# Kernel tuning notes

Hardware: AMD Instinct MI355X
Metric: run time of the kernel (lower is better)

Reference implementation:

```python
import jax, jax.numpy as jnp
import numpy as np
import math

B, C, N, L = 32, 128, 2048, 1
H, DK, APT = 8, 16, 10
EPS = 1e-5


def conv1x1(x, W, b):
    # 1x1 Conv2d on [B, C, N, L]
    return jnp.einsum('oc,bcnl->bonl', W, x) + b[None, :, None, None]


def layer_norm_12(x):
    # normalize over dims (1, 2) as in the custom LayerNorm (no affine)
    mean = x.mean(axis=(1, 2), keepdims=True)
    var = x.var(axis=(1, 2), keepdims=True)
    return (x - mean) / jnp.sqrt(var + EPS)


def setup_inputs() -> dict:
    key = jax.random.key(0)
    ks = jax.random.split(key, 10)
    s = 0.05  # small-scale init for numerical stability
    inp = {
        'input': jax.random.normal(ks[0], (B, C, N, L), jnp.float32),
        'Wq': jax.random.normal(ks[1], (C, C), jnp.float32) * s,
        'bq': jnp.zeros((C,), jnp.float32),
        'Wv': jax.random.normal(ks[2], (C, C), jnp.float32) * s,
        'bv': jnp.zeros((C,), jnp.float32),
        'Wc': jax.random.normal(ks[3], (C, C), jnp.float32) * s,
        'bc': jnp.zeros((C,), jnp.float32),
        'memory': jax.random.normal(ks[4], (H, L, N, DK), jnp.float32) * s,
        'sa_weight': jnp.ones((C, N, L), jnp.float32),
        'sa_bias': jnp.zeros((C, N, L), jnp.float32),
        'nodevec1': jax.random.normal(ks[5], (N, APT), jnp.float32),
        'nodevec2': jax.random.normal(ks[6], (APT, N), jnp.float32),
        'Wg1': jax.random.normal(ks[7], (C, C), jnp.float32) * s,
        'bg1': jnp.zeros((C,), jnp.float32),
        'Wg2': jax.random.normal(ks[8], (C, C), jnp.float32) * s,
        'bg2': jnp.zeros((C,), jnp.float32),
        'Wg3': jax.random.normal(ks[9], (C, C), jnp.float32) * s,
        'bg3': jnp.zeros((C,), jnp.float32),
    }
    return inp


def reference(input, Wq, bq, Wv, bv, Wc, bc, memory, sa_weight, sa_bias,
              nodevec1, nodevec2, Wg1, bg1, Wg2, bg2, Wg3, bg3):
    scale = math.sqrt(DK)

    def split_heads(t):  # [B,C,N,L] -> [B,H,L,N,DK]
        return t.reshape(B, H, DK, N, L).transpose(0, 1, 4, 3, 2)

    # SpatialAttention (Conv = 1x1 conv + relu; dropout off in eval)
    q = jax.nn.relu(conv1x1(input, Wq, bq))
    v = jax.nn.relu(conv1x1(input, Wv, bv))
    query = jax.nn.softmax(split_heads(q) / scale, axis=-1)     # [B,H,L,N,DK]
    value = split_heads(v)                                       # [B,H,L,N,DK]
    key = jax.nn.softmax(memory / scale, axis=-1)                # [H,L,N,DK]
    Aapt = jax.nn.softmax(jax.nn.relu(nodevec1 @ nodevec2), axis=-1)  # [N,N]

    kv = jnp.einsum('hlnx,bhlny->bhlxy', key, value)             # [B,H,L,DK,DK]
    attn_qkv = jnp.einsum('bhlnx,bhlxy->bhlny', query, kv)       # [B,H,L,N,DK]
    attn_dyn = jnp.einsum('nm,bhlnc->bhlnc', Aapt, value)        # row-sum scaling
    x = attn_qkv + attn_dyn

    # merge heads back to [B,C,N,L] and apply concat conv (Conv = conv+relu)
    x = x.transpose(0, 1, 4, 3, 2).reshape(B, C, N, L)
    x = jax.nn.relu(conv1x1(x, Wc, bc))
    x = x * sa_weight[None] + sa_bias[None] + x                  # affine branch

    # Encoder wrap
    x = x + input
    x = layer_norm_12(x)
    g = conv1x1(x, Wg1, bg1) * jax.nn.sigmoid(conv1x1(x, Wg2, bg2))
    g = conv1x1(g, Wg3, bg3)                                     # GLU
    x = g + x
    x = x * sa_weight[None] + sa_bias[None] + x
    x = layer_norm_12(x)
    return x
```

## Files before the change

kernel.cpp:

```cpp
#include <hip/hip_runtime.h>
#include <hip/hip_bf16.h>
#include <math.h>

#define DI __device__ __forceinline__

typedef short bf16x8 __attribute__((ext_vector_type(8)));
typedef float f32x4 __attribute__((ext_vector_type(4)));

constexpr int BB = 32, CC = 128, NN = 2048;
constexpr float EPSf = 1e-5f;
constexpr float RCN = 1.0f / (CC * (float)NN);

#define MFMA(a,b,c) __builtin_amdgcn_mfma_f32_16x16x32_bf16(a,b,c,0,0,0)

DI unsigned short f2b(float f){
    union { __hip_bfloat16 h; unsigned short u; } v;
    v.h = __float2bfloat16(f);
    return v.u;
}
DI float b2f(unsigned short h){
    union { unsigned u; float f; } v; v.u = ((unsigned)h) << 16;
    return v.f;
}
DI float sigm(float x){ return 1.0f / (1.0f + __expf(-x)); }

__global__ __launch_bounds__(256) void k_prep(
    const float* __restrict__ Wq, const float* __restrict__ Wv,
    const float* __restrict__ Wc, const float* __restrict__ Wg1,
    const float* __restrict__ Wg2, const float* __restrict__ Wg3,
    const float* __restrict__ mem,
    unsigned short* __restrict__ Wb, float* __restrict__ rs,
    unsigned short* __restrict__ ksT)
{
    const int tid = threadIdx.x;
    if (blockIdx.x < 96) {
        const int i = blockIdx.x * 256 + tid;
        const int m = i >> 12, q = i & 4095;
        const float* src = (m==0)?Wq:(m==1)?Wv:(m==2)?Wc:(m==3)?Wg1:(m==4)?Wg2:Wg3;
        f32x4 w = *(const f32x4*)&src[q * 4];
        ushort4 p; p.x=f2b(w[0]); p.y=f2b(w[1]); p.z=f2b(w[2]); p.w=f2b(w[3]);
        *(ushort4*)&Wb[(size_t)m * 16384 + q * 4] = p;
    } else if (blockIdx.x == 96) {
        const float* src = (tid < 128) ? Wg1 : Wg2;
        const int o = tid & 127;
        float s = 0.f;
#pragma unroll
        for (int j = 0; j < 32; j++) {
            f32x4 a = *(const f32x4*)&src[o * 128 + j * 4];
            s += a[0] + a[1] + a[2] + a[3];
        }
        rs[tid] = s;
    } else {
        const int row = (blockIdx.x - 97) * 256 + tid;
        const int h = row >> 11, n = row & 2047;
        const float* p = mem + (size_t)row * 16;
        float v[16];
        f32x4 t0 = *(const f32x4*)(p);
        f32x4 t1 = *(const f32x4*)(p + 4);
        f32x4 t2 = *(const f32x4*)(p + 8);
        f32x4 t3 = *(const f32x4*)(p + 12);
#pragma unroll
        for (int j = 0; j < 4; j++) { v[j]=t0[j]; v[4+j]=t1[j]; v[8+j]=t2[j]; v[12+j]=t3[j]; }
        float mx = v[0];
#pragma unroll
        for (int x = 1; x < 16; x++) mx = fmaxf(mx, v[x]);
        float s = 0.f;
#pragma unroll
        for (int x = 0; x < 16; x++) { v[x] = __expf((v[x] - mx) * 0.25f); s += v[x]; }
        const float is = 1.0f / s;
#pragma unroll
        for (int x = 0; x < 16; x++)
            ksT[((size_t)(h * 16 + x)) * NN + n] = f2b(v[x] * is);
    }
}

__global__ __launch_bounds__(256,2) void k_qv(
    const float* __restrict__ in, const unsigned short* __restrict__ WqB,
    const unsigned short* __restrict__ WvB, const float* __restrict__ bq,
    const float* __restrict__ bv, unsigned short* __restrict__ qT,
    unsigned short* __restrict__ vT, unsigned short* __restrict__ inT)
{
    __shared__ unsigned short tile[128 * 136];
    const int b = blockIdx.x >> 4, n0 = (blockIdx.x & 15) * 128;
    const int tid = threadIdx.x, l = tid & 63, wid = tid >> 6;
    const int wo = wid & 1, wn = wid >> 1, lr = l & 15, lg = l >> 4;
    f32x4 accq[4][4], accv[4][4];
    const f32x4 z = {0.f,0.f,0.f,0.f};
#pragma unroll
    for (int i = 0; i < 4; i++)
#pragma unroll
        for (int j = 0; j < 4; j++) { accq[i][j] = z; accv[i][j] = z; }
    const float* inb = in + (size_t)b * CC * NN;
#pragma unroll
    for (int ks = 0; ks < 4; ks++) {
        const int cb = ks * 32 + lg * 8;
        bf16x8 aq[4], av[4];
#pragma unroll
        for (int mf = 0; mf < 4; mf++) {
            const int o = wo*64 + mf*16 + lr;
            aq[mf] = *(const bf16x8*)&WqB[o * 128 + cb];
            av[mf] = *(const bf16x8*)&WvB[o * 128 + cb];
        }
        bf16x8 bx[4];
#pragma unroll
        for (int nf = 0; nf < 4; nf++) {
            const int n = n0 + wn*64 + nf*16 + lr;
            union { bf16x8 v; unsigned short u[8]; } t;
#pragma unroll
            for (int j = 0; j < 8; j++) t.u[j] = f2b(inb[(size_t)(cb + j) * NN + n]);
            bx[nf] = t.v;
        }
        if (wo == 0) {
#pragma unroll
            for (int nf = 0; nf < 4; nf++)
                *(bf16x8*)&tile[(wn*64 + nf*16 + lr) * 136 + cb] = bx[nf];
        }
#pragma unroll
        for (int mf = 0; mf < 4; mf++)
#pragma unroll
            for (int nf = 0; nf < 4; nf++) {
                accq[mf][nf] = MFMA(aq[mf], bx[nf], accq[mf][nf]);
                accv[mf][nf] = MFMA(av[mf], bx[nf], accv[mf][nf]);
            }
    }
    __syncthreads();
#pragma unroll
    for (int p = 0; p < 8; p++) {
        const int row = p*16 + (tid >> 4), col = (tid & 15) * 8;
        *(uint4*)&inT[((size_t)b * NN + n0 + row) * CC + col] =
            *(const uint4*)&tile[row * 136 + col];
    }
    __syncthreads();
#pragma unroll
    for (int mf = 0; mf < 4; mf++) {
        const int ob = wo*64 + mf*16 + lg*4;
        const f32x4 b4 = *(const f32x4*)&bq[ob];
#pragma unroll
        for (int nf = 0; nf < 4; nf++) {
            const int nl = wn*64 + nf*16 + lr;
            f32x4 a = accq[mf][nf];
            ushort4 pk;
            pk.x = f2b(fmaxf(a[0]+b4[0],0.f)); pk.y = f2b(fmaxf(a[1]+b4[1],0.f));
            pk.z = f2b(fmaxf(a[2]+b4[2],0.f)); pk.w = f2b(fmaxf(a[3]+b4[3],0.f));
            *(ushort4*)&tile[nl * 136 + ob] = pk;
        }
    }
    __syncthreads();
#pragma unroll
    for (int p = 0; p < 8; p++) {
        const int row = p*16 + (tid >> 4), col = (tid & 15) * 8;
        *(uint4*)&qT[((size_t)b * NN + n0 + row) * CC + col] =
            *(const uint4*)&tile[row * 136 + col];
    }
    __syncthreads();
#pragma unroll
    for (int mf = 0; mf < 4; mf++) {
        const int ob = wo*64 + mf*16 + lg*4;
        const f32x4 b4 = *(const f32x4*)&bv[ob];
#pragma unroll
        for (int nf = 0; nf < 4; nf++) {
            const int nl = wn*64 + nf*16 + lr;
            f32x4 a = accv[mf][nf];
            ushort4 pk;
            pk.x = f2b(fmaxf(a[0]+b4[0],0.f)); pk.y = f2b(fmaxf(a[1]+b4[1],0.f));
            pk.z = f2b(fmaxf(a[2]+b4[2],0.f)); pk.w = f2b(fmaxf(a[3]+b4[3],0.f));
            *(ushort4*)&tile[nl * 136 + ob] = pk;
        }
    }
    __syncthreads();
#pragma unroll
    for (int p = 0; p < 8; p++) {
        const int row = p*16 + (tid >> 4), col = (tid & 15) * 8;
        *(uint4*)&vT[((size_t)b * NN + n0 + row) * CC + col] =
            *(const uint4*)&tile[row * 136 + col];
    }
}

__global__ __launch_bounds__(256) void k_kv(const unsigned short* __restrict__ ksT,
                                            const unsigned short* __restrict__ vT,
                                            float* __restrict__ kvb)
{
    __shared__ unsigned short vt[4 * 16 * 520];
    __shared__ float red[1024];
    const int b = blockIdx.x >> 3, h = blockIdx.x & 7;
    const int tid = threadIdx.x, l = tid & 63, wid = tid >> 6;
    const int n0 = wid * 512;
    unsigned short* vtw = vt + wid * (16 * 520);
    const unsigned short* vb = vT + ((size_t)b * NN + n0) * CC + h * 16;
#pragma unroll
    for (int r = 0; r < 8; r++) {
        const int nl = r * 64 + l;
        uint4 q0 = *(const uint4*)&vb[(size_t)nl * CC];
        uint4 q1 = *(const uint4*)&vb[(size_t)nl * CC + 8];
        const unsigned uu[8] = {q0.x,q0.y,q0.z,q0.w,q1.x,q1.y,q1.z,q1.w};
#pragma unroll
        for (int k = 0; k < 8; k++) {
            vtw[(2*k)*520 + nl]   = (unsigned short)(uu[k] & 0xffffu);
            vtw[(2*k+1)*520 + nl] = (unsigned short)(uu[k] >> 16);
        }
    }
    const int lr = l & 15, lg = l >> 4;
    const unsigned short* ka = ksT + (size_t)h * 16 * NN;
    f32x4 acc = {0.f,0.f,0.f,0.f};
#pragma unroll
    for (int kk = 0; kk < 16; kk++) {
        bf16x8 af = *(const bf16x8*)&ka[(size_t)lr * NN + n0 + kk*32 + lg*8];
        bf16x8 bf = *(const bf16x8*)&vtw[lr * 520 + kk*32 + lg*8];
        acc = MFMA(af, bf, acc);
    }
#pragma unroll
    for (int r = 0; r < 4; r++)
        red[wid * 256 + (lg*4 + r) * 16 + lr] = acc[r];
    __syncthreads();
    {
        const float s = red[tid] + red[256 + tid] + red[512 + tid] + red[768 + tid];
        kvb[((size_t)(b * 8 + h)) * 256 + tid] = s;
    }
}

__global__ __launch_bounds__(256,2) void k_attnC(
    const unsigned short* __restrict__ qT, unsigned short* __restrict__ vT,
    const float* __restrict__ kvb, const unsigned short* __restrict__ WcB,
    const float* __restrict__ bc, const float* __restrict__ saw,
    const float* __restrict__ sab, const unsigned short* __restrict__ inT,
    float* __restrict__ part1)
{
    __shared__ float kvl[8 * 260];
    __shared__ unsigned short xc[128 * 136];
    __shared__ float red[8];
    const int b = blockIdx.x >> 4, n0 = (blockIdx.x & 15) * 128;
    const int tid = threadIdx.x;
    {
        const float* kp = kvb + (size_t)b * 2048 + (tid >> 5) * 256 + (tid & 31) * 8;
        f32x4 v0 = *(const f32x4*)kp;
        f32x4 v1 = *(const f32x4*)(kp + 4);
        float* dst = &kvl[(tid >> 5) * 260 + (tid & 31) * 8];
        *(f32x4*)dst = v0; *(f32x4*)(dst + 4) = v1;
    }
    __syncthreads();
#pragma unroll 1
    for (int it = 0; it < 4; it++) {
        const int idx = it * 256 + tid;
        const int nl = idx >> 3, h = idx & 7;
        const size_t base = ((size_t)b * NN + n0 + nl) * CC + h * 16;
        uint4 u0 = *(const uint4*)(qT + base);
        uint4 u1 = *(const uint4*)(qT + base + 8);
        uint4 w0 = *(const uint4*)(vT + base);
        uint4 w1 = *(const uint4*)(vT + base + 8);
        unsigned uu[8] = {u0.x,u0.y,u0.z,u0.w,u1.x,u1.y,u1.z,u1.w};
        float mx = -1e30f;
#pragma unroll
        for (int j = 0; j < 8; j++) {
            mx = fmaxf(mx, b2f((unsigned short)(uu[j] & 0xffffu)));
            mx = fmaxf(mx, b2f((unsigned short)(uu[j] >> 16)));
        }
        const float* kh = &kvl[h * 260];
        f32x4 r0 = {0,0,0,0}, r1 = {0,0,0,0}, r2 = {0,0,0,0}, r3 = {0,0,0,0};
        float s = 0.f;
#pragma unroll
        for (int x = 0; x < 16; x++) {
            const unsigned short qh = (x & 1) ? (unsigned short)(uu[x >> 1] >> 16)
                                              : (unsigned short)(uu[x >> 1] & 0xffffu);
            const float e = __expf((b2f(qh) - mx) * 0.25f);
            s += e;
            const f32x4 k0 = *(const f32x4*)&kh[x * 16];
            const f32x4 k1 = *(const f32x4*)&kh[x * 16 + 4];
            const f32x4 k2 = *(const f32x4*)&kh[x * 16 + 8];
            const f32x4 k3 = *(const f32x4*)&kh[x * 16 + 12];
#pragma unroll
            for (int j = 0; j < 4; j++) {
                r0[j] = fmaf(e, k0[j], r0[j]);
                r1[j] = fmaf(e, k1[j], r1[j]);
                r2[j] = fmaf(e, k2[j], r2[j]);
                r3[j] = fmaf(e, k3[j], r3[j]);
            }
        }
        const float is = 1.0f / s;
        unsigned vv[8] = {w0.x,w0.y,w0.z,w0.w,w1.x,w1.y,w1.z,w1.w};
        unsigned short* xp = &xc[nl * 136 + h * 16];
#pragma unroll
        for (int j2 = 0; j2 < 4; j2++) {
            const f32x4 rr = (j2==0)?r0:(j2==1)?r1:(j2==2)?r2:r3;
            ushort4 pk;
            pk.x = f2b(rr[0]*is + b2f((unsigned short)(vv[2*j2]   & 0xffffu)));
            pk.y = f2b(rr[1]*is + b2f((unsigned short)(vv[2*j2]   >> 16)));
            pk.z = f2b(rr[2]*is + b2f((unsigned short)(vv[2*j2+1] & 0xffffu)));
            pk.w = f2b(rr[3]*is + b2f((unsigned short)(vv[2*j2+1] >> 16)));
            *(ushort4*)&xp[j2 * 4] = pk;
        }
    }
    __syncthreads();
    const int l = tid & 63, wid = tid >> 6;
    const int wo = wid & 1, wn = wid >> 1, lr = l & 15, lg = l >> 4;
    f32x4 acc[4][4];
    const f32x4 z = {0.f,0.f,0.f,0.f};
#pragma unroll
    for (int i = 0; i < 4; i++)
#pragma unroll
        for (int j = 0; j < 4; j++) acc[i][j] = z;
#pragma unroll
    for (int ks = 0; ks < 4; ks++) {
        const int cb = ks * 32 + lg * 8;
        bf16x8 af[4];
#pragma unroll
        for (int mf = 0; mf < 4; mf++)
            af[mf] = *(const bf16x8*)&WcB[(wo*64 + mf*16 + lr) * 128 + cb];
        bf16x8 bx[4];
#pragma unroll
        for (int nf = 0; nf < 4; nf++)
            bx[nf] = *(const bf16x8*)&xc[(wn*64 + nf*16 + lr) * 136 + cb];
#pragma unroll
        for (int mf = 0; mf < 4; mf++)
#pragma unroll
            for (int nf = 0; nf < 4; nf++)
                acc[mf][nf] = MFMA(af[mf], bx[nf], acc[mf][nf]);
    }
    __syncthreads();
    float sum = 0.f, ssq = 0.f;
#pragma unroll
    for (int mf = 0; mf < 4; mf++) {
        const int ob = wo*64 + mf*16 + lg*4;
        const f32x4 b4 = *(const f32x4*)&bc[ob];
#pragma unroll
        for (int nf = 0; nf < 4; nf++) {
            const int nl = wn*64 + nf*16 + lr;
            const int n = n0 + nl;
            f32x4 a = acc[mf][nf];
            const ushort4 iu = *(const ushort4*)&inT[((size_t)b * NN + n) * CC + ob];
            float ys[4];
#pragma unroll
            for (int r = 0; r < 4; r++) {
                const int o = ob + r;
                const float t = fmaxf(a[r] + b4[r], 0.f);
                const float sw = saw[(size_t)o * NN + n];
                const float sb = sab[(size_t)o * NN + n];
                const unsigned short iv = (r==0)?iu.x:(r==1)?iu.y:(r==2)?iu.z:iu.w;
                float y = t * sw + sb + t + b2f(iv);
                sum += y; ssq += y * y;
                ys[r] = y;
            }
            ushort4 pk;
            pk.x = f2b(ys[0]); pk.y = f2b(ys[1]); pk.z = f2b(ys[2]); pk.w = f2b(ys[3]);
            *(ushort4*)&xc[nl * 136 + ob] = pk;
        }
    }
    __syncthreads();
#pragma unroll
    for (int p = 0; p < 8; p++) {
        const int row = p*16 + (tid >> 4), col = (tid & 15) * 8;
        *(uint4*)&vT[((size_t)b * NN + n0 + row) * CC + col] =
            *(const uint4*)&xc[row * 136 + col];
    }
#pragma unroll
    for (int off = 32; off > 0; off >>= 1) {
        sum += __shfl_down(sum, off);
        ssq += __shfl_down(ssq, off);
    }
    if ((tid & 63) == 0) { red[wid*2] = sum; red[wid*2+1] = ssq; }
    __syncthreads();
    if (tid == 0) {
        part1[2 * blockIdx.x]     = red[0]+red[2]+red[4]+red[6];
        part1[2 * blockIdx.x + 1] = red[1]+red[3]+red[5]+red[7];
    }
}

__global__ __launch_bounds__(256,2) void k_glu3(
    const unsigned short* __restrict__ y1,
    const unsigned short* __restrict__ W1B, const unsigned short* __restrict__ W2B,
    const unsigned short* __restrict__ W3B,
    const float* __restrict__ b1, const float* __restrict__ b2,
    const float* __restrict__ b3, const float* __restrict__ rs,
    const float* __restrict__ part1, const float* __restrict__ saw,
    const float* __restrict__ sab, unsigned short* __restrict__ X2,
    float* __restrict__ part2)
{
    __shared__ unsigned short yt[128 * 136];
    __shared__ unsigned short gx[128 * 136];
    __shared__ float cs[256];
    __shared__ float red[8];
    const int b = blockIdx.x >> 4, n0 = (blockIdx.x & 15) * 128;
    const int tid = threadIdx.x;
    float s0 = 0.f, q0 = 0.f;
#pragma unroll
    for (int t = 0; t < 16; t++) { s0 += part1[(b*16+t)*2]; q0 += part1[(b*16+t)*2+1]; }
    const float mean = s0 * RCN;
    const float var  = q0 * RCN - mean * mean;
    const float inv  = rsqrtf(var + EPSf);
    {
        const int cq = tid & 15;
#pragma unroll
        for (int it = 0; it < 8; it++) {
            const int n = it * 16 + (tid >> 4);
            uint4 u = *(const uint4*)&y1[((size_t)b * NN + n0 + n) * CC + cq * 8];
            *(uint4*)&yt[n * 136 + cq * 8] = u;
        }
    }
    {
        const int o = tid & 127;
        const float bb = (tid < 128) ? b1[o] : b2[o];
        cs[tid] = bb - mean * inv * rs[tid];
    }
    __syncthreads();
    const int l = tid & 63, wid = tid >> 6;
    const int wo = wid & 1, wn = wid >> 1, lr = l & 15, lg = l >> 4;
    {
        f32x4 acc1[4][4], acc2[4][4];
        const f32x4 z = {0.f,0.f,0.f,0.f};
#pragma unroll
        for (int i = 0; i < 4; i++)
#pragma unroll
            for (int j = 0; j < 4; j++) { acc1[i][j] = z; acc2[i][j] = z; }
#pragma unroll
        for (int ks = 0; ks < 4; ks++) {
            const int cb = ks * 32 + lg * 8;
            bf16x8 a1[4], a2[4];
#pragma unroll
            for (int mf = 0; mf < 4; mf++) {
                const int o = wo*64 + mf*16 + lr;
                a1[mf] = *(const bf16x8*)&W1B[o * 128 + cb];
                a2[mf] = *(const bf16x8*)&W2B[o * 128 + cb];
            }
            bf16x8 bx[4];
#pragma unroll
            for (int nf = 0; nf < 4; nf++)
                bx[nf] = *(const bf16x8*)&yt[(wn*64 + nf*16 + lr) * 136 + cb];
#pragma unroll
            for (int mf = 0; mf < 4; mf++)
#pragma unroll
                for (int nf = 0; nf < 4; nf++) {
                    acc1[mf][nf] = MFMA(a1[mf], bx[nf], acc1[mf][nf]);
                    acc2[mf][nf] = MFMA(a2[mf], bx[nf], acc2[mf][nf]);
                }
        }
#pragma unroll
        for (int mf = 0; mf < 4; mf++) {
            const int ob = wo*64 + mf*16 + lg*4;
            const f32x4 c1 = *(const f32x4*)&cs[ob];
            const f32x4 c2 = *(const f32x4*)&cs[128 + ob];
#pragma unroll
            for (int nf = 0; nf < 4; nf++) {
                const int nl = wn*64 + nf*16 + lr;
                ushort4 pk;
                float g1, g2;
                g1 = acc1[mf][nf][0]*inv + c1[0]; g2 = acc2[mf][nf][0]*inv + c2[0];
                pk.x = f2b(g1 * sigm(g2));
                g1 = acc1[mf][nf][1]*inv + c1[1]; g2 = acc2[mf][nf][1]*inv + c2[1];
                pk.y = f2b(g1 * sigm(g2));
                g1 = acc1[mf][nf][2]*inv + c1[2]; g2 = acc2[mf][nf][2]*inv + c2[2];
                pk.z = f2b(g1 * sigm(g2));
                g1 = acc1[mf][nf][3]*inv + c1[3]; g2 = acc2[mf][nf][3]*inv + c2[3];
                pk.w = f2b(g1 * sigm(g2));
                *(ushort4*)&gx[nl * 136 + ob] = pk;
            }
        }
    }
    __syncthreads();
    f32x4 acc[4][4];
    const f32x4 z = {0.f,0.f,0.f,0.f};
#pragma unroll
    for (int i = 0; i < 4; i++)
#pragma unroll
        for (int j = 0; j < 4; j++) acc[i][j] = z;
#pragma unroll
    for (int ks = 0; ks < 4; ks++) {
        const int cb = ks * 32 + lg * 8;
        bf16x8 af[4];
#pragma unroll
        for (int mf = 0; mf < 4; mf++)
            af[mf] = *(const bf16x8*)&W3B[(wo*64 + mf*16 + lr) * 128 + cb];
        bf16x8 bx[4];
#pragma unroll
        for (int nf = 0; nf < 4; nf++)
            bx[nf] = *(const bf16x8*)&gx[(wn*64 + nf*16 + lr) * 136 + cb];
#pragma unroll
        for (int mf = 0; mf < 4; mf++)
#pragma unroll
            for (int nf = 0; nf < 4; nf++)
                acc[mf][nf] = MFMA(af[mf], bx[nf], acc[mf][nf]);
    }
    __syncthreads();
    float sum = 0.f, ssq = 0.f;
#pragma unroll
    for (int mf = 0; mf < 4; mf++) {
        const int ob = wo*64 + mf*16 + lg*4;
        const f32x4 b4 = *(const f32x4*)&b3[ob];
#pragma unroll
        for (int nf = 0; nf < 4; nf++) {
            const int nl = wn*64 + nf*16 + lr;
            const int n = n0 + nl;
            ushort4 yq = *(const ushort4*)&yt[nl * 136 + ob];
            f32x4 a = acc[mf][nf];
            float ys[4];
#pragma unroll
            for (int r = 0; r < 4; r++) {
                const int o = ob + r;
                const unsigned short ev = (r==0)?yq.x:(r==1)?yq.y:(r==2)?yq.z:yq.w;
                const float t = a[r] + b4[r] + (b2f(ev) - mean) * inv;
                const float sw = saw[(size_t)o * NN + n];
                const float sb = sab[(size_t)o * NN + n];
                const float y = t * sw + sb + t;
                sum += y; ssq += y * y;
                ys[r] = y;
            }
            ushort4 pk;
            pk.x = f2b(ys[0]); pk.y = f2b(ys[1]); pk.z = f2b(ys[2]); pk.w = f2b(ys[3]);
            *(ushort4*)&gx[nl * 136 + ob] = pk;
        }
    }
    __syncthreads();
#pragma unroll
    for (int p = 0; p < 8; p++) {
        const int row = p*16 + (tid >> 4), col = (tid & 15) * 8;
        *(uint4*)&X2[((size_t)b * NN + n0 + row) * CC + col] =
            *(const uint4*)&gx[row * 136 + col];
    }
#pragma unroll
    for (int off = 32; off > 0; off >>= 1) {
        sum += __shfl_down(sum, off);
        ssq += __shfl_down(ssq, off);
    }
    if ((tid & 63) == 0) { red[wid*2] = sum; red[wid*2+1] = ssq; }
    __syncthreads();
    if (tid == 0) {
        part2[2 * blockIdx.x]     = red[0]+red[2]+red[4]+red[6];
        part2[2 * blockIdx.x + 1] = red[1]+red[3]+red[5]+red[7];
    }
}

__global__ __launch_bounds__(256) void k_lnfin(const unsigned short* __restrict__ x2,
                                               const float* __restrict__ part2,
                                               float* __restrict__ out)
{
    __shared__ unsigned ts[64 * 69];
    const int b = blockIdx.x >> 5, n0 = (blockIdx.x & 31) * 64;
    const int tid = threadIdx.x;
    float s0 = 0.f, q0 = 0.f;
#pragma unroll
    for (int t = 0; t < 16; t++) { s0 += part2[(b*16+t)*2]; q0 += part2[(b*16+t)*2+1]; }
    const float mean = s0 * RCN;
    const float var  = q0 * RCN - mean * mean;
    const float inv  = rsqrtf(var + EPSf);
    {
        const int n = tid >> 2, qd = tid & 3;
        const unsigned short* src = x2 + ((size_t)b * NN + n0 + n) * CC + qd * 32;
        uint4 a0 = *(const uint4*)(src);
        uint4 a1 = *(const uint4*)(src + 8);
        uint4 a2 = *(const uint4*)(src + 16);
        uint4 a3 = *(const uint4*)(src + 24);
        unsigned u[16] = {a0.x,a0.y,a0.z,a0.w, a1.x,a1.y,a1.z,a1.w,
                          a2.x,a2.y,a2.z,a2.w, a3.x,a3.y,a3.z,a3.w};
#pragma unroll
        for (int k = 0; k < 16; k++)
            ts[(qd * 16 + k) * 69 + n] = u[k];
    }
    __syncthreads();
#pragma unroll
    for (int pass = 0; pass < 8; pass++) {
        const int c = pass * 16 + (tid >> 4), nq = tid & 15;
        const int cp = c >> 1, hi = c & 1;
        f32x4 v;
#pragma unroll
        for (int j = 0; j < 4; j++) {
            const unsigned u = ts[cp * 69 + nq * 4 + j];
            const unsigned short hv = hi ? (unsigned short)(u >> 16)
                                         : (unsigned short)(u & 0xffffu);
            v[j] = (b2f(hv) - mean) * inv;
        }
        *(f32x4*)&out[((size_t)b * CC + c) * NN + n0 + nq * 4] = v;
    }
}

extern "C" void kernel_launch(void* const* d_in, const int* in_sizes, int n_in,
                              void* d_out, int out_size, void* d_ws, size_t ws_size,
                              hipStream_t stream)
{
    const float* input = (const float*)d_in[0];
    const float* Wq  = (const float*)d_in[1];
    const float* bq  = (const float*)d_in[2];
    const float* Wv  = (const float*)d_in[3];
    const float* bv  = (const float*)d_in[4];
    const float* Wc  = (const float*)d_in[5];
    const float* bc  = (const float*)d_in[6];
    const float* mem = (const float*)d_in[7];
    const float* saw = (const float*)d_in[8];
    const float* sab = (const float*)d_in[9];
    const float* Wg1 = (const float*)d_in[12];
    const float* bg1 = (const float*)d_in[13];
    const float* Wg2 = (const float*)d_in[14];
    const float* bg2 = (const float*)d_in[15];
    const float* Wg3 = (const float*)d_in[16];
    const float* bg3 = (const float*)d_in[17];
    float* out = (float*)d_out;

    unsigned char* wsb = (unsigned char*)d_ws;
    unsigned short* qT  = (unsigned short*)(wsb);
    unsigned short* vT  = (unsigned short*)(wsb + 16777216);
    unsigned short* ksT = (unsigned short*)(wsb + 33554432);
    float* kvb   = (float*)(wsb + 34078720);
    unsigned short* Wb  = (unsigned short*)(wsb + 34340864);
    float* rs    = (float*)(wsb + 34537472);
    float* part1 = (float*)(wsb + 34538496);
    float* part2 = (float*)(wsb + 34542592);
    unsigned short* inT = (unsigned short*)d_out;

    k_prep <<<161,  256, 0, stream>>>(Wq, Wv, Wc, Wg1, Wg2, Wg3, mem, Wb, rs, ksT);
    k_qv   <<<512,  256, 0, stream>>>(input, Wb, Wb + 16384, bq, bv, qT, vT, inT);
    k_kv   <<<256,  256, 0, stream>>>(ksT, vT, kvb);
    k_attnC<<<512,  256, 0, stream>>>(qT, vT, kvb, Wb + 2*16384, bc, saw, sab,
                                      inT, part1);
    k_glu3 <<<512,  256, 0, stream>>>(vT, Wb + 3*16384, Wb + 4*16384, Wb + 5*16384,
                                      bg1, bg2, bg3, rs, part1, saw, sab, qT, part2);
    k_lnfin<<<1024, 256, 0, stream>>>(qT, part2, out);
}
```

Before: 115.2 us.

## Store sa_weight/sa_bias as bf16 and relax launch bounds on GEMM kernels

Adds a prep stage that converts the per-(channel,node) affine weight and bias to bf16 in scratch space inside the output buffer. The attention-concat and GLU epilogues then read these half-size arrays instead of the fp32 originals, cutting epilogue memory traffic. It also drops the min-occupancy hint from 2 to 1 on k_qv and k_glu3, and inserts scheduling barriers in the epilogue loops. The cost is bf16 rounding of the affine parameters, extra prep-kernel work on every call, and possibly lower occupancy.

```diff
diff --git a/kernel.cpp b/kernel.cpp
--- a/kernel.cpp
+++ b/kernel.cpp
@@ -28,9 +28,11 @@
     const float* __restrict__ Wq, const float* __restrict__ Wv,
     const float* __restrict__ Wc, const float* __restrict__ Wg1,
     const float* __restrict__ Wg2, const float* __restrict__ Wg3,
-    const float* __restrict__ mem,
+    const float* __restrict__ mem, const float* __restrict__ saw,
+    const float* __restrict__ sab,
     unsigned short* __restrict__ Wb, float* __restrict__ rs,
-    unsigned short* __restrict__ ksT)
+    unsigned short* __restrict__ ksT, unsigned short* __restrict__ sawb,
+    unsigned short* __restrict__ sabb)
 {
     const int tid = threadIdx.x;
     if (blockIdx.x < 96) {
@@ -50,7 +52,7 @@
             s += a[0] + a[1] + a[2] + a[3];
         }
         rs[tid] = s;
-    } else {
+    } else if (blockIdx.x < 161) {
         const int row = (blockIdx.x - 97) * 256 + tid;
         const int h = row >> 11, n = row & 2047;
         const float* p = mem + (size_t)row * 16;
@@ -71,10 +73,18 @@
 #pragma unroll
         for (int x = 0; x < 16; x++)
             ksT[((size_t)(h * 16 + x)) * NN + n] = f2b(v[x] * is);
-    }
-}
-
-__global__ __launch_bounds__(256,2) void k_qv(
+    } else {
+        const int i = (blockIdx.x - 161) * 256 + tid;
+        const int m = i >> 16, q = i & 65535;
+        const float* src = m ? sab : saw;
+        unsigned short* dst = m ? sabb : sawb;
+        f32x4 w = *(const f32x4*)&src[q * 4];
+        ushort4 p; p.x=f2b(w[0]); p.y=f2b(w[1]); p.z=f2b(w[2]); p.w=f2b(w[3]);
+        *(ushort4*)&dst[q * 4] = p;
+    }
+}
+
+__global__ __launch_bounds__(256,1) void k_qv(
     const float* __restrict__ in, const unsigned short* __restrict__ WqB,
     const unsigned short* __restrict__ WvB, const float* __restrict__ bq,
     const float* __restrict__ bv, unsigned short* __restrict__ qT,
@@ -221,8 +231,8 @@
 __global__ __launch_bounds__(256,2) void k_attnC(
     const unsigned short* __restrict__ qT, unsigned short* __restrict__ vT,
     const float* __restrict__ kvb, const unsigned short* __restrict__ WcB,
-    const float* __restrict__ bc, const float* __restrict__ saw,
-    const float* __restrict__ sab, const unsigned short* __restrict__ inT,
+    const float* __restrict__ bc, const unsigned short* __restrict__ sawb,
+    const unsigned short* __restrict__ sabb, const unsigned short* __restrict__ inT,
     float* __restrict__ part1)
 {
     __shared__ float kvl[8 * 260];
@@ -332,8 +342,8 @@
             for (int r = 0; r < 4; r++) {
                 const int o = ob + r;
                 const float t = fmaxf(a[r] + b4[r], 0.f);
-                const float sw = saw[(size_t)o * NN + n];
-                const float sb = sab[(size_t)o * NN + n];
+                const float sw = b2f(sawb[(size_t)o * NN + n]);
+                const float sb = b2f(sabb[(size_t)o * NN + n]);
                 const unsigned short iv = (r==0)?iu.x:(r==1)?iu.y:(r==2)?iu.z:iu.w;
                 float y = t * sw + sb + t + b2f(iv);
                 sum += y; ssq += y * y;
@@ -343,6 +353,7 @@
             pk.x = f2b(ys[0]); pk.y = f2b(ys[1]); pk.z = f2b(ys[2]); pk.w = f2b(ys[3]);
             *(ushort4*)&xc[nl * 136 + ob] = pk;
         }
+        __builtin_amdgcn_sched_barrier(0);
     }
     __syncthreads();
 #pragma unroll
@@ -364,14 +375,14 @@
     }
 }
 
-__global__ __launch_bounds__(256,2) void k_glu3(
+__global__ __launch_bounds__(256,1) void k_glu3(
     const unsigned short* __restrict__ y1,
     const unsigned short* __restrict__ W1B, const unsigned short* __restrict__ W2B,
     const unsigned short* __restrict__ W3B,
     const float* __restrict__ b1, const float* __restrict__ b2,
     const float* __restrict__ b3, const float* __restrict__ rs,
-    const float* __restrict__ part1, const float* __restrict__ saw,
-    const float* __restrict__ sab, unsigned short* __restrict__ X2,
+    const float* __restrict__ part1, const unsigned short* __restrict__ sawb,
+    const unsigned short* __restrict__ sabb, unsigned short* __restrict__ X2,
     float* __restrict__ part2)
 {
     __shared__ unsigned short yt[128 * 136];
@@ -496,8 +507,8 @@
                 const int o = ob + r;
                 const unsigned short ev = (r==0)?yq.x:(r==1)?yq.y:(r==2)?yq.z:yq.w;
                 const float t = a[r] + b4[r] + (b2f(ev) - mean) * inv;
-                const float sw = saw[(size_t)o * NN + n];
-                const float sb = sab[(size_t)o * NN + n];
+                const float sw = b2f(sawb[(size_t)o * NN + n]);
+                const float sb = b2f(sabb[(size_t)o * NN + n]);
                 const float y = t * sw + sb + t;
                 sum += y; ssq += y * y;
                 ys[r] = y;
@@ -506,6 +517,7 @@
             pk.x = f2b(ys[0]); pk.y = f2b(ys[1]); pk.z = f2b(ys[2]); pk.w = f2b(ys[3]);
             *(ushort4*)&gx[nl * 136 + ob] = pk;
         }
+        __builtin_amdgcn_sched_barrier(0);
     }
     __syncthreads();
 #pragma unroll
@@ -601,14 +613,17 @@
     float* rs    = (float*)(wsb + 34537472);
     float* part1 = (float*)(wsb + 34538496);
     float* part2 = (float*)(wsb + 34542592);
-    unsigned short* inT = (unsigned short*)d_out;
-
-    k_prep <<<161,  256, 0, stream>>>(Wq, Wv, Wc, Wg1, Wg2, Wg3, mem, Wb, rs, ksT);
+    unsigned short* inT  = (unsigned short*)d_out;
+    unsigned short* sawb = (unsigned short*)((unsigned char*)d_out + 16777216);
+    unsigned short* sabb = sawb + 262144;
+
+    k_prep <<<673,  256, 0, stream>>>(Wq, Wv, Wc, Wg1, Wg2, Wg3, mem, saw, sab,
+                                      Wb, rs, ksT, sawb, sabb);
     k_qv   <<<512,  256, 0, stream>>>(input, Wb, Wb + 16384, bq, bv, qT, vT, inT);
     k_kv   <<<256,  256, 0, stream>>>(ksT, vT, kvb);
-    k_attnC<<<512,  256, 0, stream>>>(qT, vT, kvb, Wb + 2*16384, bc, saw, sab,
+    k_attnC<<<512,  256, 0, stream>>>(qT, vT, kvb, Wb + 2*16384, bc, sawb, sabb,
                                       inT, part1);
     k_glu3 <<<512,  256, 0, stream>>>(vT, Wb + 3*16384, Wb + 4*16384, Wb + 5*16384,
-                                      bg1, bg2, bg3, rs, part1, saw, sab, qT, part2);
+                                      bg1, bg2, bg3, rs, part1, sawb, sabb, qT, part2);
     k_lnfin<<<1024, 256, 0, stream>>>(qT, part2, out);
 }
```

After: 124.9 us. 1.08x slower.
